# Kernel optimization log

Measured on AMD Instinct MI355X. Metric: run time of the kernel, lower is better.

Reference implementation:

```python
import jax, jax.numpy as jnp
import numpy as np

H, D, BS = 32, 128, 64          # num_heads, head_dim, gate block_size
GATE_DIM = 64
GATE_TEMP = 2.0                 # _GATE_TARGET_TEMPERATURE
CLAMP_MIN, CLAMP_MAX = -50.0, 50.0


def _rotate_half(x):
    x1, x2 = jnp.split(x, 2, axis=-1)
    return jnp.concatenate([-x2, x1], axis=-1)


def setup_inputs() -> dict:
    key = jax.random.key(0)
    ks = jax.random.split(key, 8)
    B, S, E = 1, 2048, 4096
    hidden_states = jax.random.normal(ks[0], (B, S, E), jnp.float32) * 0.02
    # standard RoPE tables, [B, S, D]
    inv_freq = 1.0 / (10000.0 ** (jnp.arange(0, D, 2, dtype=jnp.float32) / D))
    freqs = jnp.arange(S, dtype=jnp.float32)[:, None] * inv_freq[None, :]
    emb = jnp.concatenate([freqs, freqs], axis=-1)
    cos = jnp.broadcast_to(jnp.cos(emb)[None], (B, S, D)).astype(jnp.float32)
    sin = jnp.broadcast_to(jnp.sin(emb)[None], (B, S, D)).astype(jnp.float32)
    Wq = jax.random.normal(ks[1], (E, E), jnp.float32) * 0.02
    Wk = jax.random.normal(ks[2], (E, E), jnp.float32) * 0.02
    Wv = jax.random.normal(ks[3], (E, E), jnp.float32) * 0.02
    Wo = jax.random.normal(ks[4], (E, E), jnp.float32) * 0.02
    Wg_q = jax.random.normal(ks[5], (GATE_DIM, D), jnp.float32) * 0.05
    Wg_k = jax.random.normal(ks[6], (GATE_DIM, D), jnp.float32) * 0.05
    return {"hidden_states": hidden_states, "cos": cos, "sin": sin,
            "Wq": Wq, "Wk": Wk, "Wv": Wv, "Wo": Wo,
            "Wg_q": Wg_q, "Wg_k": Wg_k}


def reference(hidden_states, cos, sin, Wq, Wk, Wv, Wo, Wg_q, Wg_k):
    B, S, E = hidden_states.shape
    scale = np.float32(1.0 / np.sqrt(D))

    # ---- base attention (training path: full dense attention w/ scores) ----
    q = (hidden_states @ Wq.T).reshape(B, S, H, D).transpose(0, 2, 1, 3)  # [B,H,S,D]
    k = (hidden_states @ Wk.T).reshape(B, S, H, D).transpose(0, 2, 1, 3)
    v = (hidden_states @ Wv.T).reshape(B, S, H, D).transpose(0, 2, 1, 3)

    # _apply_rotary_pos_emb: cos/sin are 3D [B,S,D] -> unsqueeze head dim
    c, s = cos[:, None], sin[:, None]
    q = q * c + _rotate_half(q) * s
    k = k * c + _rotate_half(k) * s

    scores = jnp.einsum('bhqd,bhkd->bhqk', q, k) * scale  # [B,H,S,S]
    causal = jnp.tril(jnp.ones((S, S), dtype=bool))
    scores = jnp.where(causal, scores, -jnp.inf)
    attn = jax.nn.softmax(scores, axis=-1)
    ctx = jnp.einsum('bhqk,bhkd->bhqd', attn, v)
    attn_output = ctx.transpose(0, 2, 1, 3).reshape(B, S, E) @ Wo.T

    # ---- _compute_gate_target: blockwise maxpool -> clamp -> tempered softmax ----
    NB = S // BS  # S divisible by BS, so the -inf padding branch is a no-op
    block_max = scores.reshape(B, H, NB, BS, NB, BS).max(axis=(3, 5))  # [B,H,NB,NB]
    finite = jnp.isfinite(block_max)
    block_max = jnp.where(finite, jnp.clip(block_max, CLAMP_MIN, CLAMP_MAX), block_max)
    gate_target = jax.nn.softmax(
        block_max.reshape(B, H, NB * NB) / GATE_TEMP, axis=-1
    ).reshape(B, H, NB, NB)

    # ---- AttnGate prediction: mean-pooled block Q/K -> low-rank block logits ----
    qb = q.reshape(B, H, NB, BS, D).mean(axis=3)  # [B,H,NB,D]
    kb = k.reshape(B, H, NB, BS, D).mean(axis=3)
    gq = jnp.einsum('bhnd,gd->bhng', qb, Wg_q)
    gk = jnp.einsum('bhnd,gd->bhng', kb, Wg_k)
    glogits = jnp.einsum('bhqg,bhkg->bhqk', gq, gk) * np.float32(1.0 / np.sqrt(GATE_DIM))
    bmask = jnp.tril(jnp.ones((NB, NB), dtype=bool))  # block-causal
    glogits = jnp.where(bmask, glogits, -jnp.inf)
    gate_pred = jax.nn.softmax(
        glogits.reshape(B, H, NB * NB), axis=-1
    ).reshape(B, H, NB, NB)

    return attn_output, gate_pred, gate_target
```

## Files before the change

### kernel.cpp

```cpp
#include <hip/hip_runtime.h>
#include <stdint.h>

#define S_LEN 2048
#define EMB   4096
#define NHEAD 32
#define DHEAD 128
#define NBLK  32
#define GDIM  64

typedef float  f32x4  __attribute__((ext_vector_type(4)));
typedef __bf16 bf16x8 __attribute__((ext_vector_type(8)));
typedef unsigned short u16;

__device__ __forceinline__ u16 f2bf(float f) {
  uint32_t u = __float_as_uint(f);
  u += 0x7fffu + ((u >> 16) & 1u);
  return (u16)(u >> 16);
}
__device__ __forceinline__ float bf2f(u16 u) {
  return __uint_as_float(((uint32_t)u) << 16);
}

__device__ __forceinline__ void ld_lds16(const u16* g, u16* l) {
  __builtin_amdgcn_global_load_lds((const __attribute__((address_space(1))) void*)g,
                                   (__attribute__((address_space(3))) void*)l, 16, 0, 0);
}

__global__ void conv_f32_bf16(const float* __restrict__ in, u16* __restrict__ out, int n4) {
  int i = blockIdx.x * 256 + threadIdx.x;
  if (i >= n4) return;
  float4 v = ((const float4*)in)[i];
  ushort4 o;
  o.x = f2bf(v.x); o.y = f2bf(v.y); o.z = f2bf(v.z); o.w = f2bf(v.w);
  ((ushort4*)out)[i] = o;
}

__global__ void conv3_f32_bf16(const float* __restrict__ a, const float* __restrict__ b,
                               const float* __restrict__ c, u16* __restrict__ oa,
                               u16* __restrict__ ob, u16* __restrict__ oc, int n4) {
  int i = blockIdx.x * 256 + threadIdx.x;
  if (i >= n4) return;
  const float* in = (blockIdx.y == 0) ? a : (blockIdx.y == 1) ? b : c;
  u16* out = (blockIdx.y == 0) ? oa : (blockIdx.y == 1) ? ob : oc;
  float4 v = ((const float4*)in)[i];
  ushort4 o;
  o.x = f2bf(v.x); o.y = f2bf(v.y); o.z = f2bf(v.z); o.w = f2bf(v.w);
  ((ushort4*)out)[i] = o;
}

__global__ void __launch_bounds__(256, 2) qkv_gemm(
    const u16* __restrict__ A, const u16* __restrict__ Bq, const u16* __restrict__ Bk,
    const u16* __restrict__ Bv, u16* __restrict__ outq, u16* __restrict__ outk,
    u16* __restrict__ outvt, const float* __restrict__ cosp, const float* __restrict__ sinp)
{
  __shared__ u16 lA[128 * 32];
  __shared__ u16 lB[128 * 32];
  __shared__ u16 lT[128 * 132];

  const int tid = threadIdx.x;
  const int w = tid >> 6, lane = tid & 63;
  const int r = lane & 15, qd = lane >> 4;
  const int nb = blockIdx.x;
  const int which = nb >> 5;
  const int h = nb & 31;
  const int m0 = blockIdx.y * 128, n0 = h * 128;
  const int K = EMB;
  const u16* B = (which == 0) ? Bq : (which == 1) ? Bk : Bv;

  f32x4 acc[2][8];
#pragma unroll
  for (int mi = 0; mi < 2; ++mi)
#pragma unroll
    for (int ni = 0; ni < 8; ++ni) acc[mi][ni] = (f32x4){0.f, 0.f, 0.f, 0.f};

  const u16* Ab = A + (size_t)(m0 + w * 16 + (lane >> 2)) * K + (lane & 3) * 8;
  const u16* Bb = B + (size_t)(n0 + w * 16 + (lane >> 2)) * K + (lane & 3) * 8;
  u16* lAb = &lA[(w * 16) * 32];
  u16* lBb = &lB[(w * 16) * 32];

  for (int k0 = 0; k0 < K; k0 += 32) {
    __syncthreads();
    ld_lds16(Ab + k0, lAb);
    ld_lds16(Ab + (size_t)64 * K + k0, lAb + 64 * 32);
    ld_lds16(Bb + k0, lBb);
    ld_lds16(Bb + (size_t)64 * K + k0, lBb + 64 * 32);
    __syncthreads();
    bf16x8 af0 = *(const bf16x8*)&lA[(w * 32 + r) * 32 + qd * 8];
    bf16x8 af1 = *(const bf16x8*)&lA[(w * 32 + 16 + r) * 32 + qd * 8];
#pragma unroll
    for (int ni = 0; ni < 8; ++ni) {
      bf16x8 bf = *(const bf16x8*)&lB[(ni * 16 + r) * 32 + qd * 8];
      acc[0][ni] = __builtin_amdgcn_mfma_f32_16x16x32_bf16(af0, bf, acc[0][ni], 0, 0, 0);
      acc[1][ni] = __builtin_amdgcn_mfma_f32_16x16x32_bf16(af1, bf, acc[1][ni], 0, 0, 0);
    }
  }

  if (which < 2) {
    u16* out = which ? outk : outq;
#pragma unroll
    for (int mi = 0; mi < 2; ++mi)
#pragma unroll
      for (int ni = 0; ni < 4; ++ni)
#pragma unroll
        for (int rg = 0; rg < 4; ++rg) {
          int srow = m0 + w * 32 + mi * 16 + qd * 4 + rg;
          int dlo = ni * 16 + r;
          float c = cosp[srow * DHEAD + dlo];
          float s = sinp[srow * DHEAD + dlo];
          float lo = acc[mi][ni][rg], hi = acc[mi][ni + 4][rg];
          size_t base = ((size_t)h * S_LEN + srow) * DHEAD;
          out[base + dlo]      = f2bf(lo * c - hi * s);
          out[base + dlo + 64] = f2bf(hi * c + lo * s);
        }
  } else {
#pragma unroll
    for (int mi = 0; mi < 2; ++mi)
#pragma unroll
      for (int ni = 0; ni < 8; ++ni)
#pragma unroll
        for (int rg = 0; rg < 4; ++rg) {
          int sl = w * 32 + mi * 16 + qd * 4 + rg;
          lT[sl * 132 + ni * 16 + r] = f2bf(acc[mi][ni][rg]);
        }
    __syncthreads();
    const int d = tid >> 1, sh = (tid & 1) * 64;
    size_t obase = ((size_t)h * DHEAD + d) * S_LEN + m0 + sh;
#pragma unroll
    for (int i8 = 0; i8 < 8; ++i8) {
      u16 tmp[8];
#pragma unroll
      for (int j = 0; j < 8; ++j) tmp[j] = lT[(sh + i8 * 8 + j) * 132 + d];
      *(uint4*)&outvt[obase + i8 * 8] = *(uint4*)tmp;
    }
  }
}

__global__ void __launch_bounds__(256, 2) gemm_out(
    const u16* __restrict__ A, const u16* __restrict__ B, float* __restrict__ out)
{
  __shared__ u16 lA[128 * 32];
  __shared__ u16 lB[128 * 32];
  const int tid = threadIdx.x;
  const int w = tid >> 6, lane = tid & 63;
  const int r = lane & 15, qd = lane >> 4;
  const int m0 = blockIdx.y * 128, n0 = blockIdx.x * 128;
  const int K = EMB;

  f32x4 acc[2][8];
#pragma unroll
  for (int mi = 0; mi < 2; ++mi)
#pragma unroll
    for (int ni = 0; ni < 8; ++ni) acc[mi][ni] = (f32x4){0.f, 0.f, 0.f, 0.f};

  const u16* Ab = A + (size_t)(m0 + w * 16 + (lane >> 2)) * K + (lane & 3) * 8;
  const u16* Bb = B + (size_t)(n0 + w * 16 + (lane >> 2)) * K + (lane & 3) * 8;
  u16* lAb = &lA[(w * 16) * 32];
  u16* lBb = &lB[(w * 16) * 32];

  for (int k0 = 0; k0 < K; k0 += 32) {
    __syncthreads();
    ld_lds16(Ab + k0, lAb);
    ld_lds16(Ab + (size_t)64 * K + k0, lAb + 64 * 32);
    ld_lds16(Bb + k0, lBb);
    ld_lds16(Bb + (size_t)64 * K + k0, lBb + 64 * 32);
    __syncthreads();
    bf16x8 af0 = *(const bf16x8*)&lA[(w * 32 + r) * 32 + qd * 8];
    bf16x8 af1 = *(const bf16x8*)&lA[(w * 32 + 16 + r) * 32 + qd * 8];
#pragma unroll
    for (int ni = 0; ni < 8; ++ni) {
      bf16x8 bf = *(const bf16x8*)&lB[(ni * 16 + r) * 32 + qd * 8];
      acc[0][ni] = __builtin_amdgcn_mfma_f32_16x16x32_bf16(af0, bf, acc[0][ni], 0, 0, 0);
      acc[1][ni] = __builtin_amdgcn_mfma_f32_16x16x32_bf16(af1, bf, acc[1][ni], 0, 0, 0);
    }
  }
#pragma unroll
  for (int mi = 0; mi < 2; ++mi)
#pragma unroll
    for (int ni = 0; ni < 8; ++ni)
#pragma unroll
      for (int rg = 0; rg < 4; ++rg) {
        int srow = m0 + w * 32 + mi * 16 + qd * 4 + rg;
        out[(size_t)srow * EMB + n0 + ni * 16 + r] = acc[mi][ni][rg];
      }
}

__global__ void __launch_bounds__(256, 2) attn_fwd(
    const u16* __restrict__ qg, const u16* __restrict__ kg, const u16* __restrict__ vtg,
    u16* __restrict__ ctx, float* __restrict__ bmax)
{
  __shared__ u16 lK[64 * 132];
  __shared__ u16 lV[128 * 76];
  __shared__ u16 lP[64 * 76];
  __shared__ float lBM[4 * NBLK];

  const int tid = threadIdx.x;
  const int w = tid >> 6, lane = tid & 63;
  const int r = lane & 15, qd = lane >> 4;
  const int h = blockIdx.y;
  const u16* ksrc = kg + (size_t)h * S_LEN * DHEAD;
  const u16* vsrc = vtg + (size_t)h * DHEAD * S_LEN;
  const float scale = 0.08838834764831845f;

  for (int qsel = 0; qsel < 2; ++qsel) {
    const int qb = qsel ? (31 - (int)blockIdx.x) : (int)blockIdx.x;

    bf16x8 qf[4];
    {
      const u16* qp = qg + ((size_t)h * S_LEN + qb * 64 + w * 16 + r) * DHEAD + qd * 8;
#pragma unroll
      for (int ki = 0; ki < 4; ++ki) qf[ki] = *(const bf16x8*)(qp + ki * 32);
    }

    f32x4 o[8];
#pragma unroll
    for (int dt = 0; dt < 8; ++dt) o[dt] = (f32x4){0.f, 0.f, 0.f, 0.f};
    float m_run[4], l_run[4];
#pragma unroll
    for (int rg = 0; rg < 4; ++rg) { m_run[rg] = -__builtin_inff(); l_run[rg] = 0.f; }

    for (int kb = 0; kb <= qb; ++kb) {
      __syncthreads();
#pragma unroll
      for (int i = 0; i < 4; ++i) {
        int c = tid + 256 * i;
        int row = c >> 4, col = (c & 15) * 8;
        *(uint4*)&lK[row * 132 + col] = *(const uint4*)(ksrc + (size_t)(kb * 64 + row) * DHEAD + col);
      }
#pragma unroll
      for (int i = 0; i < 4; ++i) {
        int c = tid + 256 * i;
        int row = c >> 3, col = (c & 7) * 8;
        *(uint4*)&lV[row * 76 + col] = *(const uint4*)(vsrc + (size_t)row * S_LEN + kb * 64 + col);
      }
      __syncthreads();

      f32x4 sf[4];
#pragma unroll
      for (int nt = 0; nt < 4; ++nt) sf[nt] = (f32x4){0.f, 0.f, 0.f, 0.f};
#pragma unroll
      for (int ki = 0; ki < 4; ++ki)
#pragma unroll
        for (int nt = 0; nt < 4; ++nt) {
          bf16x8 bf = *(const bf16x8*)&lK[(nt * 16 + r) * 132 + ki * 32 + qd * 8];
          sf[nt] = __builtin_amdgcn_mfma_f32_16x16x32_bf16(qf[ki], bf, sf[nt], 0, 0, 0);
        }

      float rmax[4];
#pragma unroll
      for (int rg = 0; rg < 4; ++rg) rmax[rg] = -__builtin_inff();
#pragma unroll
      for (int nt = 0; nt < 4; ++nt)
#pragma unroll
        for (int rg = 0; rg < 4; ++rg) {
          float s = sf[nt][rg] * scale;
          if (kb == qb) {
            int col = nt * 16 + r, row = w * 16 + qd * 4 + rg;
            if (col > row) s = -__builtin_inff();
          }
          sf[nt][rg] = s;
          rmax[rg] = fmaxf(rmax[rg], s);
        }
#pragma unroll
      for (int rg = 0; rg < 4; ++rg) {
        float v = rmax[rg];
        v = fmaxf(v, __shfl_xor(v, 1));
        v = fmaxf(v, __shfl_xor(v, 2));
        v = fmaxf(v, __shfl_xor(v, 4));
        v = fmaxf(v, __shfl_xor(v, 8));
        rmax[rg] = v;
      }
      {
        float v = fmaxf(fmaxf(rmax[0], rmax[1]), fmaxf(rmax[2], rmax[3]));
        v = fmaxf(v, __shfl_xor(v, 16));
        v = fmaxf(v, __shfl_xor(v, 32));
        if (lane == 0) lBM[w * NBLK + kb] = v;
      }

      float alpha[4], rsum[4];
#pragma unroll
      for (int rg = 0; rg < 4; ++rg) {
        float mn = fmaxf(m_run[rg], rmax[rg]);
        alpha[rg] = __expf(m_run[rg] - mn);
        m_run[rg] = mn;
        rsum[rg] = 0.f;
      }
#pragma unroll
      for (int nt = 0; nt < 4; ++nt)
#pragma unroll
        for (int rg = 0; rg < 4; ++rg) {
          float p = __expf(sf[nt][rg] - m_run[rg]);
          sf[nt][rg] = p;
          rsum[rg] += p;
        }
#pragma unroll
      for (int rg = 0; rg < 4; ++rg) {
        float v = rsum[rg];
        v += __shfl_xor(v, 1);
        v += __shfl_xor(v, 2);
        v += __shfl_xor(v, 4);
        v += __shfl_xor(v, 8);
        l_run[rg] = l_run[rg] * alpha[rg] + v;
      }
#pragma unroll
      for (int nt = 0; nt < 4; ++nt)
#pragma unroll
        for (int rg = 0; rg < 4; ++rg)
          lP[(w * 16 + qd * 4 + rg) * 76 + nt * 16 + r] = f2bf(sf[nt][rg]);
#pragma unroll
      for (int dt = 0; dt < 8; ++dt)
#pragma unroll
        for (int rg = 0; rg < 4; ++rg) o[dt][rg] *= alpha[rg];
      bf16x8 pa0 = *(const bf16x8*)&lP[(w * 16 + r) * 76 + qd * 8];
      bf16x8 pa1 = *(const bf16x8*)&lP[(w * 16 + r) * 76 + 32 + qd * 8];
#pragma unroll
      for (int dt = 0; dt < 8; ++dt) {
        bf16x8 bv0 = *(const bf16x8*)&lV[(dt * 16 + r) * 76 + qd * 8];
        bf16x8 bv1 = *(const bf16x8*)&lV[(dt * 16 + r) * 76 + 32 + qd * 8];
        o[dt] = __builtin_amdgcn_mfma_f32_16x16x32_bf16(pa0, bv0, o[dt], 0, 0, 0);
        o[dt] = __builtin_amdgcn_mfma_f32_16x16x32_bf16(pa1, bv1, o[dt], 0, 0, 0);
      }
    }

    float inv[4];
#pragma unroll
    for (int rg = 0; rg < 4; ++rg) inv[rg] = 1.f / l_run[rg];
#pragma unroll
    for (int dt = 0; dt < 8; ++dt)
#pragma unroll
      for (int rg = 0; rg < 4; ++rg) {
        int srow = qb * 64 + w * 16 + qd * 4 + rg;
        ctx[(size_t)srow * EMB + h * DHEAD + dt * 16 + r] = f2bf(o[dt][rg] * inv[rg]);
      }
    __syncthreads();
    if (tid <= qb) {
      float v = fmaxf(fmaxf(lBM[0 * NBLK + tid], lBM[1 * NBLK + tid]),
                      fmaxf(lBM[2 * NBLK + tid], lBM[3 * NBLK + tid]));
      bmax[((size_t)h * NBLK + qb) * NBLK + tid] = v;
    }
  }
}

__global__ void bmean2(const u16* __restrict__ q, const u16* __restrict__ k,
                       float* __restrict__ qo, float* __restrict__ ko) {
  int nb = blockIdx.x, h = blockIdx.y, t = threadIdx.x;
  const u16* x = blockIdx.z ? k : q;
  float* out = blockIdx.z ? ko : qo;
  const u16* p = x + ((size_t)h * S_LEN + nb * 64) * DHEAD + t * 2;
  float s0 = 0.f, s1 = 0.f;
#pragma unroll 8
  for (int i = 0; i < 64; ++i) {
    uint32_t v = *(const uint32_t*)(p + (size_t)i * DHEAD);
    s0 += bf2f((u16)v);
    s1 += bf2f((u16)(v >> 16));
  }
  float2 rr = {s0 * (1.f / 64.f), s1 * (1.f / 64.f)};
  *(float2*)&out[((size_t)h * NBLK + nb) * DHEAD + t * 2] = rr;
}

__global__ void __launch_bounds__(256) gate_kernel(
    const float* __restrict__ qm, const float* __restrict__ km,
    const float* __restrict__ Wgq, const float* __restrict__ Wgk,
    const float* __restrict__ bmx, float* __restrict__ gpred, float* __restrict__ gtgt)
{
  __shared__ float gq[NBLK * GDIM], gk[NBLK * GDIM];
  __shared__ float red[256];
  const int h = blockIdx.x, tid = threadIdx.x;

  for (int i = 0; i < 8; ++i) {
    int e = tid + 256 * i;
    int n = e >> 6, g = e & 63;
    const float* qrow = qm + ((size_t)h * NBLK + n) * DHEAD;
    const float* krow = km + ((size_t)h * NBLK + n) * DHEAD;
    const float* wq = Wgq + g * DHEAD;
    const float* wk = Wgk + g * DHEAD;
    float s1 = 0.f, s2 = 0.f;
    for (int d = 0; d < DHEAD; ++d) { s1 += qrow[d] * wq[d]; s2 += krow[d] * wk[d]; }
    gq[e] = s1; gk[e] = s2;
  }
  __syncthreads();

  float gl[4];
  for (int i = 0; i < 4; ++i) {
    int idx = tid + 256 * i;
    int qn = idx >> 5, kn = idx & 31;
    if (kn <= qn) {
      float s = 0.f;
      for (int g = 0; g < GDIM; ++g) s += gq[qn * GDIM + g] * gk[kn * GDIM + g];
      gl[i] = s * 0.125f;
    } else gl[i] = -__builtin_inff();
  }
  float mx = fmaxf(fmaxf(gl[0], gl[1]), fmaxf(gl[2], gl[3]));
  red[tid] = mx; __syncthreads();
  for (int st = 128; st > 0; st >>= 1) { if (tid < st) red[tid] = fmaxf(red[tid], red[tid + st]); __syncthreads(); }
  float gmax = red[0]; __syncthreads();
  float ex[4], lsum = 0.f;
  for (int i = 0; i < 4; ++i) { ex[i] = __expf(gl[i] - gmax); lsum += ex[i]; }
  red[tid] = lsum; __syncthreads();
  for (int st = 128; st > 0; st >>= 1) { if (tid < st) red[tid] += red[tid + st]; __syncthreads(); }
  float invs = 1.f / red[0]; __syncthreads();
  for (int i = 0; i < 4; ++i) gpred[(size_t)h * 1024 + tid + 256 * i] = ex[i] * invs;

  float tl[4];
  for (int i = 0; i < 4; ++i) {
    int idx = tid + 256 * i;
    int qn = idx >> 5, kn = idx & 31;
    tl[i] = (kn <= qn) ? fminf(fmaxf(bmx[(size_t)h * 1024 + idx], -50.f), 50.f) * 0.5f
                       : -__builtin_inff();
  }
  float mx2 = fmaxf(fmaxf(tl[0], tl[1]), fmaxf(tl[2], tl[3]));
  red[tid] = mx2; __syncthreads();
  for (int st = 128; st > 0; st >>= 1) { if (tid < st) red[tid] = fmaxf(red[tid], red[tid + st]); __syncthreads(); }
  float tmax = red[0]; __syncthreads();
  float ex2[4], ls2 = 0.f;
  for (int i = 0; i < 4; ++i) { ex2[i] = __expf(tl[i] - tmax); ls2 += ex2[i]; }
  red[tid] = ls2; __syncthreads();
  for (int st = 128; st > 0; st >>= 1) { if (tid < st) red[tid] += red[tid + st]; __syncthreads(); }
  float inv2 = 1.f / red[0];
  for (int i = 0; i < 4; ++i) gtgt[(size_t)h * 1024 + tid + 256 * i] = ex2[i] * inv2;
}

extern "C" void kernel_launch(void* const* d_in, const int* in_sizes, int n_in,
                              void* d_out, int out_size, void* d_ws, size_t ws_size,
                              hipStream_t stream) {
  const float* hidden = (const float*)d_in[0];
  const float* cosp   = (const float*)d_in[1];
  const float* sinp   = (const float*)d_in[2];
  const float* Wq     = (const float*)d_in[3];
  const float* Wk     = (const float*)d_in[4];
  const float* Wv     = (const float*)d_in[5];
  const float* Wo     = (const float*)d_in[6];
  const float* Wgq    = (const float*)d_in[7];
  const float* Wgk    = (const float*)d_in[8];

  char* ws = (char*)d_ws;
  u16* wqb = (u16*)ws;
  u16* wkb = (u16*)(ws + 33554432);
  u16* hid = (u16*)(ws + 67108864);
  u16* qbf = (u16*)(ws + 83886080);
  u16* kbf = (u16*)(ws + 100663296);
  u16* vtb = (u16*)(ws + 117440512);
  float* bmx = (float*)(ws + 33554432);
  float* qmn = (float*)(ws + 33554432 + 131072);
  float* kmn = (float*)(ws + 33554432 + 655360);
  u16* ctx = hid;
  u16* wvb = (u16*)d_out;

  float* attn_out = (float*)d_out;
  float* gpred = attn_out + (size_t)S_LEN * EMB;
  float* gtgt  = gpred + NHEAD * NBLK * NBLK;

  conv3_f32_bf16<<<dim3(16384, 3), 256, 0, stream>>>(Wq, Wk, Wv, wqb, wkb, wvb, 4194304);
  conv_f32_bf16<<<8192, 256, 0, stream>>>(hidden, hid, 2097152);

  qkv_gemm<<<dim3(96, 16), 256, 0, stream>>>(hid, wqb, wkb, wvb, qbf, kbf, vtb, cosp, sinp);

  conv_f32_bf16<<<16384, 256, 0, stream>>>(Wo, wqb, 4194304);

  attn_fwd<<<dim3(16, NHEAD), 256, 0, stream>>>(qbf, kbf, vtb, ctx, bmx);

  bmean2<<<dim3(NBLK, NHEAD, 2), 128, 0, stream>>>(qbf, kbf, qmn, kmn);
  gate_kernel<<<NHEAD, 256, 0, stream>>>(qmn, kmn, Wgq, Wgk, bmx, gpred, gtgt);

  gemm_out<<<dim3(32, 16), 256, 0, stream>>>(ctx, wqb, attn_out);
}
```

Measured before the change: 790.6 us.

## Tile attention over 128-row query blocks with prefetch; split-K output projection

The attention kernel now gives each workgroup 128 query rows (two 64-row sub-tiles), so every K/V tile loaded into shared memory serves twice as many queries. The next K/V tile is prefetched into registers while the current one is computed, and the LDS strides change. The grid is reordered heads-first, with the heaviest query blocks scheduled first. The output projection GEMM is split over K into two halves that write separate buffers, then summed by a new add kernel, which doubles the GEMM's parallelism but adds an extra fp32 read/write pass and more register pressure.

```diff
diff --git a/kernel.cpp b/kernel.cpp
--- a/kernel.cpp
+++ b/kernel.cpp
@@ -136,7 +136,8 @@
 }
 
 __global__ void __launch_bounds__(256, 2) gemm_out(
-    const u16* __restrict__ A, const u16* __restrict__ B, float* __restrict__ out)
+    const u16* __restrict__ A, const u16* __restrict__ B,
+    float* __restrict__ out0, float* __restrict__ out1)
 {
   __shared__ u16 lA[128 * 32];
   __shared__ u16 lB[128 * 32];
@@ -145,6 +146,8 @@
   const int r = lane & 15, qd = lane >> 4;
   const int m0 = blockIdx.y * 128, n0 = blockIdx.x * 128;
   const int K = EMB;
+  const int koff = blockIdx.z * (EMB / 2);
+  float* out = blockIdx.z ? out1 : out0;
 
   f32x4 acc[2][8];
 #pragma unroll
@@ -152,12 +155,12 @@
 #pragma unroll
     for (int ni = 0; ni < 8; ++ni) acc[mi][ni] = (f32x4){0.f, 0.f, 0.f, 0.f};
 
-  const u16* Ab = A + (size_t)(m0 + w * 16 + (lane >> 2)) * K + (lane & 3) * 8;
-  const u16* Bb = B + (size_t)(n0 + w * 16 + (lane >> 2)) * K + (lane & 3) * 8;
+  const u16* Ab = A + (size_t)(m0 + w * 16 + (lane >> 2)) * K + (lane & 3) * 8 + koff;
+  const u16* Bb = B + (size_t)(n0 + w * 16 + (lane >> 2)) * K + (lane & 3) * 8 + koff;
   u16* lAb = &lA[(w * 16) * 32];
   u16* lBb = &lB[(w * 16) * 32];
 
-  for (int k0 = 0; k0 < K; k0 += 32) {
+  for (int k0 = 0; k0 < EMB / 2; k0 += 32) {
     __syncthreads();
     ld_lds16(Ab + k0, lAb);
     ld_lds16(Ab + (size_t)64 * K + k0, lAb + 64 * 32);
@@ -184,67 +187,101 @@
       }
 }
 
+__global__ void add_out(float* __restrict__ dst, const float* __restrict__ src, int n4) {
+  int i = blockIdx.x * 256 + threadIdx.x;
+  if (i >= n4) return;
+  float4 a = ((const float4*)dst)[i];
+  float4 b = ((const float4*)src)[i];
+  a.x += b.x; a.y += b.y; a.z += b.z; a.w += b.w;
+  ((float4*)dst)[i] = a;
+}
+
 __global__ void __launch_bounds__(256, 2) attn_fwd(
     const u16* __restrict__ qg, const u16* __restrict__ kg, const u16* __restrict__ vtg,
     u16* __restrict__ ctx, float* __restrict__ bmax)
 {
-  __shared__ u16 lK[64 * 132];
-  __shared__ u16 lV[128 * 76];
-  __shared__ u16 lP[64 * 76];
-  __shared__ float lBM[4 * NBLK];
+  __shared__ u16 lK[64 * 136];
+  __shared__ u16 lV[128 * 72];
+  __shared__ u16 lP[128 * 72];
+  __shared__ float lBM[2 * 4 * NBLK];
 
   const int tid = threadIdx.x;
   const int w = tid >> 6, lane = tid & 63;
   const int r = lane & 15, qd = lane >> 4;
-  const int h = blockIdx.y;
+  const int h = blockIdx.x;
+  const int qsb = 15 - (int)blockIdx.y;
+  const int kmax = 2 * qsb + 1;
+
   const u16* ksrc = kg + (size_t)h * S_LEN * DHEAD;
   const u16* vsrc = vtg + (size_t)h * DHEAD * S_LEN;
   const float scale = 0.08838834764831845f;
 
-  for (int qsel = 0; qsel < 2; ++qsel) {
-    const int qb = qsel ? (31 - (int)blockIdx.x) : (int)blockIdx.x;
-
-    bf16x8 qf[4];
-    {
-      const u16* qp = qg + ((size_t)h * S_LEN + qb * 64 + w * 16 + r) * DHEAD + qd * 8;
-#pragma unroll
-      for (int ki = 0; ki < 4; ++ki) qf[ki] = *(const bf16x8*)(qp + ki * 32);
-    }
-
-    f32x4 o[8];
-#pragma unroll
-    for (int dt = 0; dt < 8; ++dt) o[dt] = (f32x4){0.f, 0.f, 0.f, 0.f};
-    float m_run[4], l_run[4];
-#pragma unroll
-    for (int rg = 0; rg < 4; ++rg) { m_run[rg] = -__builtin_inff(); l_run[rg] = 0.f; }
-
-    for (int kb = 0; kb <= qb; ++kb) {
-      __syncthreads();
-#pragma unroll
-      for (int i = 0; i < 4; ++i) {
-        int c = tid + 256 * i;
-        int row = c >> 4, col = (c & 15) * 8;
-        *(uint4*)&lK[row * 132 + col] = *(const uint4*)(ksrc + (size_t)(kb * 64 + row) * DHEAD + col);
-      }
-#pragma unroll
-      for (int i = 0; i < 4; ++i) {
-        int c = tid + 256 * i;
-        int row = c >> 3, col = (c & 7) * 8;
-        *(uint4*)&lV[row * 76 + col] = *(const uint4*)(vsrc + (size_t)row * S_LEN + kb * 64 + col);
-      }
-      __syncthreads();
-
-      f32x4 sf[4];
-#pragma unroll
-      for (int nt = 0; nt < 4; ++nt) sf[nt] = (f32x4){0.f, 0.f, 0.f, 0.f};
-#pragma unroll
-      for (int ki = 0; ki < 4; ++ki)
-#pragma unroll
-        for (int nt = 0; nt < 4; ++nt) {
-          bf16x8 bf = *(const bf16x8*)&lK[(nt * 16 + r) * 132 + ki * 32 + qd * 8];
-          sf[nt] = __builtin_amdgcn_mfma_f32_16x16x32_bf16(qf[ki], bf, sf[nt], 0, 0, 0);
-        }
-
+  bf16x8 qf[2][4];
+#pragma unroll
+  for (int mi = 0; mi < 2; ++mi) {
+    const u16* qp = qg + ((size_t)h * S_LEN + qsb * 128 + mi * 64 + w * 16 + r) * DHEAD + qd * 8;
+#pragma unroll
+    for (int ki = 0; ki < 4; ++ki) qf[mi][ki] = *(const bf16x8*)(qp + ki * 32);
+  }
+
+  f32x4 o[2][8];
+#pragma unroll
+  for (int mi = 0; mi < 2; ++mi)
+#pragma unroll
+    for (int dt = 0; dt < 8; ++dt) o[mi][dt] = (f32x4){0.f, 0.f, 0.f, 0.f};
+  float m_run[2][4], l_run[2][4];
+#pragma unroll
+  for (int mi = 0; mi < 2; ++mi)
+#pragma unroll
+    for (int rg = 0; rg < 4; ++rg) { m_run[mi][rg] = -__builtin_inff(); l_run[mi][rg] = 0.f; }
+
+  const int kr0 = tid >> 4, kc = (tid & 15) * 8;
+  const int vr0 = tid >> 3, vc = (tid & 7) * 8;
+
+  uint4 pk[4], pv[4];
+  {
+    const u16* kp = ksrc;
+    const u16* vp = vsrc;
+#pragma unroll
+    for (int i = 0; i < 4; ++i) pk[i] = *(const uint4*)(kp + (size_t)(kr0 + 16 * i) * DHEAD + kc);
+#pragma unroll
+    for (int i = 0; i < 4; ++i) pv[i] = *(const uint4*)(vp + (size_t)(vr0 + 32 * i) * S_LEN + vc);
+  }
+
+  for (int kb = 0; kb <= kmax; ++kb) {
+    __syncthreads();
+#pragma unroll
+    for (int i = 0; i < 4; ++i) *(uint4*)&lK[(kr0 + 16 * i) * 136 + kc] = pk[i];
+#pragma unroll
+    for (int i = 0; i < 4; ++i) *(uint4*)&lV[(vr0 + 32 * i) * 72 + vc] = pv[i];
+    __syncthreads();
+    if (kb < kmax) {
+      const u16* kp = ksrc + (size_t)(kb + 1) * 64 * DHEAD;
+      const u16* vp = vsrc + (kb + 1) * 64;
+#pragma unroll
+      for (int i = 0; i < 4; ++i) pk[i] = *(const uint4*)(kp + (size_t)(kr0 + 16 * i) * DHEAD + kc);
+#pragma unroll
+      for (int i = 0; i < 4; ++i) pv[i] = *(const uint4*)(vp + (size_t)(vr0 + 32 * i) * S_LEN + vc);
+    }
+
+    f32x4 sf[2][4];
+#pragma unroll
+    for (int mi = 0; mi < 2; ++mi)
+#pragma unroll
+      for (int nt = 0; nt < 4; ++nt) sf[mi][nt] = (f32x4){0.f, 0.f, 0.f, 0.f};
+#pragma unroll
+    for (int ki = 0; ki < 4; ++ki)
+#pragma unroll
+      for (int nt = 0; nt < 4; ++nt) {
+        bf16x8 bf = *(const bf16x8*)&lK[(nt * 16 + r) * 136 + ki * 32 + qd * 8];
+        sf[0][nt] = __builtin_amdgcn_mfma_f32_16x16x32_bf16(qf[0][ki], bf, sf[0][nt], 0, 0, 0);
+        sf[1][nt] = __builtin_amdgcn_mfma_f32_16x16x32_bf16(qf[1][ki], bf, sf[1][nt], 0, 0, 0);
+      }
+
+    float alpha[2][4];
+#pragma unroll
+    for (int mi = 0; mi < 2; ++mi) {
+      const int mt = kb - 2 * qsb - mi;
       float rmax[4];
 #pragma unroll
       for (int rg = 0; rg < 4; ++rg) rmax[rg] = -__builtin_inff();
@@ -252,12 +289,13 @@
       for (int nt = 0; nt < 4; ++nt)
 #pragma unroll
         for (int rg = 0; rg < 4; ++rg) {
-          float s = sf[nt][rg] * scale;
-          if (kb == qb) {
-            int col = nt * 16 + r, row = w * 16 + qd * 4 + rg;
+          float s = sf[mi][nt][rg] * scale;
+          if (mt >= 0) {
+            int col = mt * 64 + nt * 16 + r;
+            int row = w * 16 + qd * 4 + rg;
             if (col > row) s = -__builtin_inff();
           }
-          sf[nt][rg] = s;
+          sf[mi][nt][rg] = s;
           rmax[rg] = fmaxf(rmax[rg], s);
         }
 #pragma unroll
@@ -273,23 +311,22 @@
         float v = fmaxf(fmaxf(rmax[0], rmax[1]), fmaxf(rmax[2], rmax[3]));
         v = fmaxf(v, __shfl_xor(v, 16));
         v = fmaxf(v, __shfl_xor(v, 32));
-        if (lane == 0) lBM[w * NBLK + kb] = v;
-      }
-
-      float alpha[4], rsum[4];
+        if (lane == 0) lBM[(mi * 4 + w) * NBLK + kb] = v;
+      }
+      float rsum[4];
 #pragma unroll
       for (int rg = 0; rg < 4; ++rg) {
-        float mn = fmaxf(m_run[rg], rmax[rg]);
-        alpha[rg] = __expf(m_run[rg] - mn);
-        m_run[rg] = mn;
+        float mn = fmaxf(m_run[mi][rg], rmax[rg]);
+        alpha[mi][rg] = __expf(m_run[mi][rg] - mn);
+        m_run[mi][rg] = mn;
         rsum[rg] = 0.f;
       }
 #pragma unroll
       for (int nt = 0; nt < 4; ++nt)
 #pragma unroll
         for (int rg = 0; rg < 4; ++rg) {
-          float p = __expf(sf[nt][rg] - m_run[rg]);
-          sf[nt][rg] = p;
+          float p = __expf(sf[mi][nt][rg] - m_run[mi][rg]);
+          sf[mi][nt][rg] = p;
           rsum[rg] += p;
         }
 #pragma unroll
@@ -299,43 +336,58 @@
         v += __shfl_xor(v, 2);
         v += __shfl_xor(v, 4);
         v += __shfl_xor(v, 8);
-        l_run[rg] = l_run[rg] * alpha[rg] + v;
+        l_run[mi][rg] = l_run[mi][rg] * alpha[mi][rg] + v;
       }
 #pragma unroll
       for (int nt = 0; nt < 4; ++nt)
 #pragma unroll
         for (int rg = 0; rg < 4; ++rg)
-          lP[(w * 16 + qd * 4 + rg) * 76 + nt * 16 + r] = f2bf(sf[nt][rg]);
+          lP[(mi * 64 + w * 16 + qd * 4 + rg) * 72 + nt * 16 + r] = f2bf(sf[mi][nt][rg]);
 #pragma unroll
       for (int dt = 0; dt < 8; ++dt)
 #pragma unroll
-        for (int rg = 0; rg < 4; ++rg) o[dt][rg] *= alpha[rg];
-      bf16x8 pa0 = *(const bf16x8*)&lP[(w * 16 + r) * 76 + qd * 8];
-      bf16x8 pa1 = *(const bf16x8*)&lP[(w * 16 + r) * 76 + 32 + qd * 8];
-#pragma unroll
-      for (int dt = 0; dt < 8; ++dt) {
-        bf16x8 bv0 = *(const bf16x8*)&lV[(dt * 16 + r) * 76 + qd * 8];
-        bf16x8 bv1 = *(const bf16x8*)&lV[(dt * 16 + r) * 76 + 32 + qd * 8];
-        o[dt] = __builtin_amdgcn_mfma_f32_16x16x32_bf16(pa0, bv0, o[dt], 0, 0, 0);
-        o[dt] = __builtin_amdgcn_mfma_f32_16x16x32_bf16(pa1, bv1, o[dt], 0, 0, 0);
-      }
-    }
-
+        for (int rg = 0; rg < 4; ++rg) o[mi][dt][rg] *= alpha[mi][rg];
+    }
+
+    bf16x8 pa[2][2];
+#pragma unroll
+    for (int mi = 0; mi < 2; ++mi) {
+      pa[mi][0] = *(const bf16x8*)&lP[(mi * 64 + w * 16 + r) * 72 + qd * 8];
+      pa[mi][1] = *(const bf16x8*)&lP[(mi * 64 + w * 16 + r) * 72 + 32 + qd * 8];
+    }
+#pragma unroll
+    for (int dt = 0; dt < 8; ++dt) {
+      bf16x8 bv0 = *(const bf16x8*)&lV[(dt * 16 + r) * 72 + qd * 8];
+      bf16x8 bv1 = *(const bf16x8*)&lV[(dt * 16 + r) * 72 + 32 + qd * 8];
+#pragma unroll
+      for (int mi = 0; mi < 2; ++mi) {
+        o[mi][dt] = __builtin_amdgcn_mfma_f32_16x16x32_bf16(pa[mi][0], bv0, o[mi][dt], 0, 0, 0);
+        o[mi][dt] = __builtin_amdgcn_mfma_f32_16x16x32_bf16(pa[mi][1], bv1, o[mi][dt], 0, 0, 0);
+      }
+    }
+  }
+
+#pragma unroll
+  for (int mi = 0; mi < 2; ++mi) {
     float inv[4];
 #pragma unroll
-    for (int rg = 0; rg < 4; ++rg) inv[rg] = 1.f / l_run[rg];
+    for (int rg = 0; rg < 4; ++rg) inv[rg] = 1.f / l_run[mi][rg];
 #pragma unroll
     for (int dt = 0; dt < 8; ++dt)
 #pragma unroll
       for (int rg = 0; rg < 4; ++rg) {
-        int srow = qb * 64 + w * 16 + qd * 4 + rg;
-        ctx[(size_t)srow * EMB + h * DHEAD + dt * 16 + r] = f2bf(o[dt][rg] * inv[rg]);
-      }
-    __syncthreads();
-    if (tid <= qb) {
-      float v = fmaxf(fmaxf(lBM[0 * NBLK + tid], lBM[1 * NBLK + tid]),
-                      fmaxf(lBM[2 * NBLK + tid], lBM[3 * NBLK + tid]));
-      bmax[((size_t)h * NBLK + qb) * NBLK + tid] = v;
+        int srow = qsb * 128 + mi * 64 + w * 16 + qd * 4 + rg;
+        ctx[(size_t)srow * EMB + h * DHEAD + dt * 16 + r] = f2bf(o[mi][dt][rg] * inv[rg]);
+      }
+  }
+  __syncthreads();
+  if (tid < 64) {
+    int mi = tid >> 5, kb = tid & 31;
+    int qb = 2 * qsb + mi;
+    if (kb <= qb) {
+      float v = fmaxf(fmaxf(lBM[(mi * 4 + 0) * NBLK + kb], lBM[(mi * 4 + 1) * NBLK + kb]),
+                      fmaxf(lBM[(mi * 4 + 2) * NBLK + kb], lBM[(mi * 4 + 3) * NBLK + kb]));
+      bmax[((size_t)h * NBLK + qb) * NBLK + kb] = v;
     }
   }
 }
@@ -444,6 +496,7 @@
   float* kmn = (float*)(ws + 33554432 + 655360);
   u16* ctx = hid;
   u16* wvb = (u16*)d_out;
+  float* part1 = (float*)qbf;
 
   float* attn_out = (float*)d_out;
   float* gpred = attn_out + (size_t)S_LEN * EMB;
@@ -456,10 +509,11 @@
 
   conv_f32_bf16<<<16384, 256, 0, stream>>>(Wo, wqb, 4194304);
 
-  attn_fwd<<<dim3(16, NHEAD), 256, 0, stream>>>(qbf, kbf, vtb, ctx, bmx);
+  attn_fwd<<<dim3(32, 16), 256, 0, stream>>>(qbf, kbf, vtb, ctx, bmx);
 
   bmean2<<<dim3(NBLK, NHEAD, 2), 128, 0, stream>>>(qbf, kbf, qmn, kmn);
   gate_kernel<<<NHEAD, 256, 0, stream>>>(qmn, kmn, Wgq, Wgk, bmx, gpred, gtgt);
 
-  gemm_out<<<dim3(32, 16), 256, 0, stream>>>(ctx, wqb, attn_out);
-}
+  gemm_out<<<dim3(32, 16, 2), 256, 0, stream>>>(ctx, wqb, attn_out, part1);
+  add_out<<<8192, 256, 0, stream>>>(attn_out, part1, 2097152);
+}
```

New measurement: 860.1 us. 8.8% more time.

## Load K/V fragments directly from global in attention; split-K output GEMM

Applied to the files above, without the earlier changes.

The attention kernel no longer stages K and V tiles through shared memory. Each lane loads its MFMA operands straight from global memory, which removes two barriers per key block, and the grid is reordered so the head index is the fastest-varying dimension. The output projection GEMM is split into two K-halves to double the number of workgroups, writing a partial result into a scratch buffer, and a new add kernel sums the halves. The costs are redundant uncoalesced global loads of K/V across waves, which now rely on cache, plus an extra 32MB partial write and read and one more kernel launch.

```diff
diff --git a/kernel.cpp b/kernel.cpp
--- a/kernel.cpp
+++ b/kernel.cpp
@@ -136,7 +136,8 @@
 }
 
 __global__ void __launch_bounds__(256, 2) gemm_out(
-    const u16* __restrict__ A, const u16* __restrict__ B, float* __restrict__ out)
+    const u16* __restrict__ A, const u16* __restrict__ B,
+    float* __restrict__ out0, float* __restrict__ out1)
 {
   __shared__ u16 lA[128 * 32];
   __shared__ u16 lB[128 * 32];
@@ -145,6 +146,8 @@
   const int r = lane & 15, qd = lane >> 4;
   const int m0 = blockIdx.y * 128, n0 = blockIdx.x * 128;
   const int K = EMB;
+  const int koff = blockIdx.z * (EMB / 2);
+  float* out = blockIdx.z ? out1 : out0;
 
   f32x4 acc[2][8];
 #pragma unroll
@@ -152,12 +155,12 @@
 #pragma unroll
     for (int ni = 0; ni < 8; ++ni) acc[mi][ni] = (f32x4){0.f, 0.f, 0.f, 0.f};
 
-  const u16* Ab = A + (size_t)(m0 + w * 16 + (lane >> 2)) * K + (lane & 3) * 8;
-  const u16* Bb = B + (size_t)(n0 + w * 16 + (lane >> 2)) * K + (lane & 3) * 8;
+  const u16* Ab = A + (size_t)(m0 + w * 16 + (lane >> 2)) * K + (lane & 3) * 8 + koff;
+  const u16* Bb = B + (size_t)(n0 + w * 16 + (lane >> 2)) * K + (lane & 3) * 8 + koff;
   u16* lAb = &lA[(w * 16) * 32];
   u16* lBb = &lB[(w * 16) * 32];
 
-  for (int k0 = 0; k0 < K; k0 += 32) {
+  for (int k0 = 0; k0 < EMB / 2; k0 += 32) {
     __syncthreads();
     ld_lds16(Ab + k0, lAb);
     ld_lds16(Ab + (size_t)64 * K + k0, lAb + 64 * 32);
@@ -184,25 +187,34 @@
       }
 }
 
+__global__ void add_out(float* __restrict__ dst, const float* __restrict__ src, int n4) {
+  int i = blockIdx.x * 256 + threadIdx.x;
+  if (i >= n4) return;
+  float4 a = ((const float4*)dst)[i];
+  float4 b = ((const float4*)src)[i];
+  a.x += b.x; a.y += b.y; a.z += b.z; a.w += b.w;
+  ((float4*)dst)[i] = a;
+}
+
 __global__ void __launch_bounds__(256, 2) attn_fwd(
     const u16* __restrict__ qg, const u16* __restrict__ kg, const u16* __restrict__ vtg,
     u16* __restrict__ ctx, float* __restrict__ bmax)
 {
-  __shared__ u16 lK[64 * 132];
-  __shared__ u16 lV[128 * 76];
-  __shared__ u16 lP[64 * 76];
-  __shared__ float lBM[4 * NBLK];
+  __shared__ u16 lP[64 * 72];
+  __shared__ float lBM[2 * 4 * NBLK];
 
   const int tid = threadIdx.x;
   const int w = tid >> 6, lane = tid & 63;
   const int r = lane & 15, qd = lane >> 4;
-  const int h = blockIdx.y;
+  const int h = blockIdx.x;
+  const int p = blockIdx.y;
+
   const u16* ksrc = kg + (size_t)h * S_LEN * DHEAD;
   const u16* vsrc = vtg + (size_t)h * DHEAD * S_LEN;
   const float scale = 0.08838834764831845f;
 
-  for (int qsel = 0; qsel < 2; ++qsel) {
-    const int qb = qsel ? (31 - (int)blockIdx.x) : (int)blockIdx.x;
+  for (int half = 0; half < 2; ++half) {
+    const int qb = half ? (31 - p) : p;
 
     bf16x8 qf[4];
     {
@@ -219,20 +231,8 @@
     for (int rg = 0; rg < 4; ++rg) { m_run[rg] = -__builtin_inff(); l_run[rg] = 0.f; }
 
     for (int kb = 0; kb <= qb; ++kb) {
-      __syncthreads();
-#pragma unroll
-      for (int i = 0; i < 4; ++i) {
-        int c = tid + 256 * i;
-        int row = c >> 4, col = (c & 15) * 8;
-        *(uint4*)&lK[row * 132 + col] = *(const uint4*)(ksrc + (size_t)(kb * 64 + row) * DHEAD + col);
-      }
-#pragma unroll
-      for (int i = 0; i < 4; ++i) {
-        int c = tid + 256 * i;
-        int row = c >> 3, col = (c & 7) * 8;
-        *(uint4*)&lV[row * 76 + col] = *(const uint4*)(vsrc + (size_t)row * S_LEN + kb * 64 + col);
-      }
-      __syncthreads();
+      const u16* kp = ksrc + (size_t)kb * 64 * DHEAD + r * DHEAD + qd * 8;
+      const u16* vp = vsrc + (size_t)r * S_LEN + kb * 64 + qd * 8;
 
       f32x4 sf[4];
 #pragma unroll
@@ -241,8 +241,8 @@
       for (int ki = 0; ki < 4; ++ki)
 #pragma unroll
         for (int nt = 0; nt < 4; ++nt) {
-          bf16x8 bf = *(const bf16x8*)&lK[(nt * 16 + r) * 132 + ki * 32 + qd * 8];
-          sf[nt] = __builtin_amdgcn_mfma_f32_16x16x32_bf16(qf[ki], bf, sf[nt], 0, 0, 0);
+          bf16x8 kf = *(const bf16x8*)(kp + (size_t)(nt * 16) * DHEAD + ki * 32);
+          sf[nt] = __builtin_amdgcn_mfma_f32_16x16x32_bf16(qf[ki], kf, sf[nt], 0, 0, 0);
         }
 
       float rmax[4];
@@ -273,7 +273,7 @@
         float v = fmaxf(fmaxf(rmax[0], rmax[1]), fmaxf(rmax[2], rmax[3]));
         v = fmaxf(v, __shfl_xor(v, 16));
         v = fmaxf(v, __shfl_xor(v, 32));
-        if (lane == 0) lBM[w * NBLK + kb] = v;
+        if (lane == 0) lBM[(half * 4 + w) * NBLK + kb] = v;
       }
 
       float alpha[4], rsum[4];
@@ -288,9 +288,9 @@
       for (int nt = 0; nt < 4; ++nt)
 #pragma unroll
         for (int rg = 0; rg < 4; ++rg) {
-          float p = __expf(sf[nt][rg] - m_run[rg]);
-          sf[nt][rg] = p;
-          rsum[rg] += p;
+          float ps = __expf(sf[nt][rg] - m_run[rg]);
+          sf[nt][rg] = ps;
+          rsum[rg] += ps;
         }
 #pragma unroll
       for (int rg = 0; rg < 4; ++rg) {
@@ -305,17 +305,17 @@
       for (int nt = 0; nt < 4; ++nt)
 #pragma unroll
         for (int rg = 0; rg < 4; ++rg)
-          lP[(w * 16 + qd * 4 + rg) * 76 + nt * 16 + r] = f2bf(sf[nt][rg]);
+          lP[(w * 16 + qd * 4 + rg) * 72 + nt * 16 + r] = f2bf(sf[nt][rg]);
 #pragma unroll
       for (int dt = 0; dt < 8; ++dt)
 #pragma unroll
         for (int rg = 0; rg < 4; ++rg) o[dt][rg] *= alpha[rg];
-      bf16x8 pa0 = *(const bf16x8*)&lP[(w * 16 + r) * 76 + qd * 8];
-      bf16x8 pa1 = *(const bf16x8*)&lP[(w * 16 + r) * 76 + 32 + qd * 8];
+      bf16x8 pa0 = *(const bf16x8*)&lP[(w * 16 + r) * 72 + qd * 8];
+      bf16x8 pa1 = *(const bf16x8*)&lP[(w * 16 + r) * 72 + 32 + qd * 8];
 #pragma unroll
       for (int dt = 0; dt < 8; ++dt) {
-        bf16x8 bv0 = *(const bf16x8*)&lV[(dt * 16 + r) * 76 + qd * 8];
-        bf16x8 bv1 = *(const bf16x8*)&lV[(dt * 16 + r) * 76 + 32 + qd * 8];
+        bf16x8 bv0 = *(const bf16x8*)(vp + (size_t)(dt * 16) * S_LEN);
+        bf16x8 bv1 = *(const bf16x8*)(vp + (size_t)(dt * 16) * S_LEN + 32);
         o[dt] = __builtin_amdgcn_mfma_f32_16x16x32_bf16(pa0, bv0, o[dt], 0, 0, 0);
         o[dt] = __builtin_amdgcn_mfma_f32_16x16x32_bf16(pa1, bv1, o[dt], 0, 0, 0);
       }
@@ -331,11 +331,16 @@
         int srow = qb * 64 + w * 16 + qd * 4 + rg;
         ctx[(size_t)srow * EMB + h * DHEAD + dt * 16 + r] = f2bf(o[dt][rg] * inv[rg]);
       }
-    __syncthreads();
-    if (tid <= qb) {
-      float v = fmaxf(fmaxf(lBM[0 * NBLK + tid], lBM[1 * NBLK + tid]),
-                      fmaxf(lBM[2 * NBLK + tid], lBM[3 * NBLK + tid]));
-      bmax[((size_t)h * NBLK + qb) * NBLK + tid] = v;
+  }
+
+  __syncthreads();
+  if (tid < 64) {
+    int half = tid >> 5, kb = tid & 31;
+    int qb = half ? (31 - p) : p;
+    if (kb <= qb) {
+      float v = fmaxf(fmaxf(lBM[(half * 4 + 0) * NBLK + kb], lBM[(half * 4 + 1) * NBLK + kb]),
+                      fmaxf(lBM[(half * 4 + 2) * NBLK + kb], lBM[(half * 4 + 3) * NBLK + kb]));
+      bmax[((size_t)h * NBLK + qb) * NBLK + kb] = v;
     }
   }
 }
@@ -444,6 +449,7 @@
   float* kmn = (float*)(ws + 33554432 + 655360);
   u16* ctx = hid;
   u16* wvb = (u16*)d_out;
+  float* part1 = (float*)qbf;
 
   float* attn_out = (float*)d_out;
   float* gpred = attn_out + (size_t)S_LEN * EMB;
@@ -456,10 +462,11 @@
 
   conv_f32_bf16<<<16384, 256, 0, stream>>>(Wo, wqb, 4194304);
 
-  attn_fwd<<<dim3(16, NHEAD), 256, 0, stream>>>(qbf, kbf, vtb, ctx, bmx);
+  attn_fwd<<<dim3(32, 16), 256, 0, stream>>>(qbf, kbf, vtb, ctx, bmx);
 
   bmean2<<<dim3(NBLK, NHEAD, 2), 128, 0, stream>>>(qbf, kbf, qmn, kmn);
   gate_kernel<<<NHEAD, 256, 0, stream>>>(qmn, kmn, Wgq, Wgk, bmx, gpred, gtgt);
 
-  gemm_out<<<dim3(32, 16), 256, 0, stream>>>(ctx, wqb, attn_out);
-}
+  gemm_out<<<dim3(32, 16, 2), 256, 0, stream>>>(ctx, wqb, attn_out, part1);
+  add_out<<<8192, 256, 0, stream>>>(attn_out, part1, 2097152);
+}
```

Measured after the change: 959.6 us. +21.4%, slower.
